# Kernel tuning notes

Hardware: AMD Instinct MI355X
Metric: run time of the kernel (lower is better)

Reference implementation:

```python
import jax, jax.numpy as jnp
import numpy as np

N_NODES = 50000
N_EDGES = 800000
N_GRAPHS = 512
NUM_TYPES = 1000
EMB = 128
HID = 128


def setup_inputs() -> dict:
    key = jax.random.key(0)
    ks = jax.random.split(key, 8)
    x_type = jax.random.randint(ks[0], (N_NODES,), 0, NUM_TYPES, dtype=jnp.int32)
    edge_index = jax.random.randint(ks[1], (2, N_EDGES), 0, N_NODES, dtype=jnp.int32)
    batch = jnp.sort(jax.random.randint(ks[2], (N_NODES,), 0, N_GRAPHS, dtype=jnp.int32))
    emb = jax.random.normal(ks[3], (NUM_TYPES, EMB), jnp.float32)
    s1 = 1.0 / np.sqrt(EMB)
    s2 = 1.0 / np.sqrt(HID)
    W1 = jax.random.normal(ks[4], (EMB, HID), jnp.float32) * s1
    b1 = jnp.zeros((HID,), jnp.float32)
    W2 = jax.random.normal(ks[5], (HID, HID), jnp.float32) * s2
    b2 = jnp.zeros((HID,), jnp.float32)
    return {"x_type": x_type, "edge_index": edge_index, "batch": batch,
            "emb": emb, "W1": W1, "b1": b1, "W2": W2, "b2": b2}


def _gcn_norm(edge_index, n_nodes):
    # PyG GCNConv default: add self-loops, symmetric normalization.
    loops = jnp.arange(n_nodes, dtype=edge_index.dtype)
    src = jnp.concatenate([edge_index[0], loops])  # [E+N]
    dst = jnp.concatenate([edge_index[1], loops])
    deg = jax.ops.segment_sum(jnp.ones_like(dst, jnp.float32), dst, num_segments=n_nodes)
    dis = jax.lax.rsqrt(deg)  # deg >= 1 thanks to self-loops
    norm = dis[src] * dis[dst]  # [E+N]
    return src, dst, norm


def _gcn_conv(x, src, dst, norm, W, b, n_nodes):
    h = x @ W                                  # [N, out]
    msg = h[src] * norm[:, None]               # edge-gathered, normalized messages
    out = jax.ops.segment_sum(msg, dst, num_segments=n_nodes)  # scatter-add
    return out + b


def reference(x_type, edge_index, batch, emb, W1, b1, W2, b2):
    src, dst, norm = _gcn_norm(edge_index, N_NODES)
    x = emb[x_type]                            # [N, EMB]
    x = jax.nn.relu(_gcn_conv(x, src, dst, norm, W1, b1, N_NODES))
    x = _gcn_conv(x, src, dst, norm, W2, b2, N_NODES)
    # index_add_ pooling over graphs (dropout is identity in eval / p=0)
    out = jax.ops.segment_sum(x, batch, num_segments=N_GRAPHS)  # [G, HID]
    return out
```

## Files before the change

### kernel.cpp

```cpp
#include <hip/hip_runtime.h>

#define N_NODES 50000
#define N_EDGES 800000
#define N_GRAPHS 512
#define FDIM 128
#define NTYPES_PAD 1000

#define NBLK 128
#define CHUNK ((N_EDGES + NBLK - 1) / NBLK)
#define NQUAD (N_NODES / 4)
#define NSB ((NQUAD + 255) / 256)
#define EMBW_BLOCKS 16
#define NPW 2
#define NW ((N_NODES + NPW - 1) / NPW)

typedef __bf16 bf16x8 __attribute__((ext_vector_type(8)));
typedef float f32x4 __attribute__((ext_vector_type(4)));
union BF8 { bf16x8 v; unsigned short u[8]; };

__device__ __forceinline__ unsigned short f2bf(float f) {
  unsigned int u = __float_as_uint(f);
  unsigned int r = (u + 0x7FFFu + ((u >> 16) & 1u)) >> 16;
  return (unsigned short)r;
}
__device__ __forceinline__ float bflo(unsigned int v) {
  return __uint_as_float(v << 16);
}
__device__ __forceinline__ float bfhi(unsigned int v) {
  return __uint_as_float(v & 0xFFFF0000u);
}

__global__ __launch_bounds__(512) void k_hist(const int* __restrict__ dst,
                                              unsigned int* __restrict__ Hist,
                                              unsigned char* __restrict__ rank8,
                                              int* __restrict__ g_done) {
  __shared__ unsigned int h[NQUAD];
  int b = blockIdx.x, t = threadIdx.x;
  if (b == 0 && t == 0) *g_done = 0;
  for (int i = t; i < NQUAD; i += 512) h[i] = 0;
  __syncthreads();
  int e0 = b * CHUNK, e1 = min(e0 + CHUNK, N_EDGES);
  for (int e = e0 + t; e < e1; e += 512) {
    int d = dst[e];
    unsigned int sh = (d & 3) * 8;
    unsigned int old = atomicAdd(&h[d >> 2], 1u << sh);
    rank8[e] = (unsigned char)((old >> sh) & 0xFFu);
  }
  __syncthreads();
  unsigned int* H = Hist + (size_t)b * NQUAD;
  for (int i = t; i < NQUAD; i += 512) H[i] = h[i];
}

__global__ __launch_bounds__(256) void k_prep(
    const unsigned int* __restrict__ Hist, const int* __restrict__ batch,
    unsigned int* __restrict__ Cur, float* __restrict__ dis,
    int* __restrict__ row_ptr, float* __restrict__ Zb,
    int* __restrict__ gstart, int* __restrict__ g_bsum,
    int* __restrict__ g_done, const float* __restrict__ emb,
    const float* __restrict__ W1, unsigned short* __restrict__ T1) {
  __shared__ unsigned short sh[16384];
  int blk = blockIdx.x, tid = threadIdx.x;

  if (blk >= NSB) {
    unsigned short* Ws = sh;
    int t = tid, w = t >> 6, l = t & 63;
    for (int i = t; i < 16384; i += 256) {
      int k = i >> 7, n = i & 127;
      Ws[n * 128 + (k ^ ((n & 15) << 3))] = f2bf(W1[i]);
    }
    int row0 = (blk - NSB) * 64 + w * 16;
    int arow = row0 + (l & 15);
    bool ok = arow < NTYPES_PAD;
    bf16x8 a[4];
#pragma unroll
    for (int ks = 0; ks < 4; ++ks) {
      BF8 av;
      const float* ap = emb + (size_t)arow * FDIM + (l >> 4) * 8 + ks * 32;
#pragma unroll
      for (int i = 0; i < 8; ++i) av.u[i] = ok ? f2bf(ap[i]) : 0;
      a[ks] = av.v;
    }
    __syncthreads();
    f32x4 acc[8] = {};
#pragma unroll
    for (int ks = 0; ks < 4; ++ks) {
#pragma unroll
      for (int ct = 0; ct < 8; ++ct) {
        int n = ct * 16 + (l & 15);
        int kk = (ks * 32 + (l >> 4) * 8) ^ ((n & 15) << 3);
        bf16x8 b = *(const bf16x8*)&Ws[n * 128 + kk];
        acc[ct] =
            __builtin_amdgcn_mfma_f32_16x16x32_bf16(a[ks], b, acc[ct], 0, 0, 0);
      }
    }
#pragma unroll
    for (int ct = 0; ct < 8; ++ct) {
      int col = ct * 16 + (l & 15);
#pragma unroll
      for (int r = 0; r < 4; ++r) {
        int row = row0 + (l >> 4) * 4 + r;
        if (row < NTYPES_PAD) T1[row * FDIM + col] = f2bf(acc[ct][r]);
      }
    }
    return;
  }

  int* si = (int*)sh;
  int q = blk * 256 + tid;

  for (int i = blk * 256 + tid; i < N_GRAPHS * FDIM; i += NSB * 256)
    Zb[i] = 0.0f;

  if (q < NQUAD) {
    int i0 = 4 * q;
    int prev = (i0 == 0) ? -1 : batch[i0 - 1];
#pragma unroll
    for (int k = 0; k < 4; ++k) {
      int i = i0 + k;
      int bb = batch[i];
      for (int g = prev + 1; g <= bb; ++g) gstart[g] = i;
      prev = bb;
    }
    if (i0 + 3 == N_NODES - 1)
      for (int g = prev + 1; g <= N_GRAPHS; ++g) gstart[g] = N_NODES;
  }

  unsigned int r0 = 0, r1 = 0, r2 = 0, r3 = 0;
  if (q < NQUAD) {
    for (int b = 0; b < NBLK; ++b) {
      unsigned int v = Hist[(size_t)b * NQUAD + q];
      Cur[(size_t)b * NQUAD + q] =
          (r0 & 255u) | ((r1 & 255u) << 8) | ((r2 & 255u) << 16) | (r3 << 24);
      r0 += v & 255u;
      r1 += (v >> 8) & 255u;
      r2 += (v >> 16) & 255u;
      r3 += v >> 24;
    }
    float4 dv = make_float4(rsqrtf((float)r0 + 1.f), rsqrtf((float)r1 + 1.f),
                            rsqrtf((float)r2 + 1.f), rsqrtf((float)r3 + 1.f));
    ((float4*)dis)[q] = dv;
  }

  int tsum = (q < NQUAD) ? (int)(r0 + r1 + r2 + r3) : 0;
  si[tid] = tsum;
  __syncthreads();
  for (int d = 1; d < 256; d <<= 1) {
    int u = (tid >= d) ? si[tid - d] : 0;
    __syncthreads();
    si[tid] += u;
    __syncthreads();
  }
  int excl = si[tid] - tsum;
  int btotal = si[255];

  if (tid == 0) {
    atomicExch(&g_bsum[blk], btotal);
    __threadfence();
    atomicAdd(g_done, 1);
    while (atomicAdd(g_done, 0) < NSB) {
    }
  }
  __syncthreads();
  int* sb = si + 256;
  if (tid < NSB) sb[tid] = atomicAdd(&g_bsum[tid], 0);
  __syncthreads();
  int bpref = 0;
  for (int t = 0; t < blk; ++t) bpref += sb[t];

  if (q < NQUAD) {
    int base = bpref + excl;
    ((int4*)row_ptr)[q] =
        make_int4(base, base + (int)r0, base + (int)(r0 + r1),
                  base + (int)(r0 + r1 + r2));
  }
  if (q == NQUAD - 1) row_ptr[N_NODES] = N_EDGES;
}

__global__ __launch_bounds__(512) void k_fill2(
    const int* __restrict__ src, const int* __restrict__ dst,
    const int* __restrict__ x_type, const int* __restrict__ row_ptr,
    const unsigned int* __restrict__ Cur, const unsigned char* __restrict__ rank8,
    const float* __restrict__ dis, unsigned long long* __restrict__ csr) {
  int e = blockIdx.x * blockDim.x + threadIdx.x;
  if (e >= N_EDGES) return;
  int b = e / CHUNK;
  int s = src[e], d = dst[e];
  unsigned int cw = Cur[(size_t)b * NQUAD + (d >> 2)];
  int base = (int)((cw >> ((d & 3) * 8)) & 0xFFu);
  int pos = row_ptr[d] + base + (int)rank8[e];
  unsigned int lo = (unsigned int)s | ((unsigned int)x_type[s] << 16);
  unsigned int hi = (unsigned int)f2bf(dis[d]);
  csr[pos] = (unsigned long long)lo | ((unsigned long long)hi << 32);
}

__global__ void k_agg1(const int* __restrict__ x_type,
                       const unsigned short* __restrict__ T1,
                       const float* __restrict__ b1,
                       const int* __restrict__ row_ptr,
                       const unsigned long long* __restrict__ csr,
                       const float* __restrict__ dis,
                       unsigned int* __restrict__ y1) {
  int gid = blockIdx.x * blockDim.x + threadIdx.x;
  int node = gid >> 6;
  int lane = gid & 63;
  if (node >= N_NODES) return;
  const unsigned int* T = (const unsigned int*)T1;
  const unsigned int* C = (const unsigned int*)csr;
  float di = dis[node];
  unsigned int v = T[(size_t)x_type[node] * 64 + lane];
  float ax = bflo(v) * di, ay = bfhi(v) * di;
  int j = row_ptr[node], end = row_ptr[node + 1];
  for (; j + 8 <= end; j += 8) {
    unsigned int e0 = C[2 * j], e1 = C[2 * j + 2];
    unsigned int e2 = C[2 * j + 4], e3 = C[2 * j + 6];
    unsigned int e4 = C[2 * j + 8], e5 = C[2 * j + 10];
    unsigned int e6 = C[2 * j + 12], e7 = C[2 * j + 14];
    unsigned int u0 = T[(size_t)(e0 >> 16) * 64 + lane];
    unsigned int u1 = T[(size_t)(e1 >> 16) * 64 + lane];
    unsigned int u2 = T[(size_t)(e2 >> 16) * 64 + lane];
    unsigned int u3 = T[(size_t)(e3 >> 16) * 64 + lane];
    unsigned int u4 = T[(size_t)(e4 >> 16) * 64 + lane];
    unsigned int u5 = T[(size_t)(e5 >> 16) * 64 + lane];
    unsigned int u6 = T[(size_t)(e6 >> 16) * 64 + lane];
    unsigned int u7 = T[(size_t)(e7 >> 16) * 64 + lane];
    float n0 = dis[e0 & 0xFFFFu], n1 = dis[e1 & 0xFFFFu];
    float n2 = dis[e2 & 0xFFFFu], n3 = dis[e3 & 0xFFFFu];
    float n4 = dis[e4 & 0xFFFFu], n5 = dis[e5 & 0xFFFFu];
    float n6 = dis[e6 & 0xFFFFu], n7 = dis[e7 & 0xFFFFu];
    ax = fmaf(bflo(u0), n0, ax); ay = fmaf(bfhi(u0), n0, ay);
    ax = fmaf(bflo(u1), n1, ax); ay = fmaf(bfhi(u1), n1, ay);
    ax = fmaf(bflo(u2), n2, ax); ay = fmaf(bfhi(u2), n2, ay);
    ax = fmaf(bflo(u3), n3, ax); ay = fmaf(bfhi(u3), n3, ay);
    ax = fmaf(bflo(u4), n4, ax); ay = fmaf(bfhi(u4), n4, ay);
    ax = fmaf(bflo(u5), n5, ax); ay = fmaf(bfhi(u5), n5, ay);
    ax = fmaf(bflo(u6), n6, ax); ay = fmaf(bfhi(u6), n6, ay);
    ax = fmaf(bflo(u7), n7, ax); ay = fmaf(bfhi(u7), n7, ay);
  }
  for (; j + 4 <= end; j += 4) {
    unsigned int e0 = C[2 * j], e1 = C[2 * j + 2];
    unsigned int e2 = C[2 * j + 4], e3 = C[2 * j + 6];
    unsigned int u0 = T[(size_t)(e0 >> 16) * 64 + lane];
    unsigned int u1 = T[(size_t)(e1 >> 16) * 64 + lane];
    unsigned int u2 = T[(size_t)(e2 >> 16) * 64 + lane];
    unsigned int u3 = T[(size_t)(e3 >> 16) * 64 + lane];
    float n0 = dis[e0 & 0xFFFFu], n1 = dis[e1 & 0xFFFFu];
    float n2 = dis[e2 & 0xFFFFu], n3 = dis[e3 & 0xFFFFu];
    ax = fmaf(bflo(u0), n0, ax); ay = fmaf(bfhi(u0), n0, ay);
    ax = fmaf(bflo(u1), n1, ax); ay = fmaf(bfhi(u1), n1, ay);
    ax = fmaf(bflo(u2), n2, ax); ay = fmaf(bfhi(u2), n2, ay);
    ax = fmaf(bflo(u3), n3, ax); ay = fmaf(bfhi(u3), n3, ay);
  }
  for (; j < end; ++j) {
    unsigned int e = C[2 * j];
    unsigned int u = T[(size_t)(e >> 16) * 64 + lane];
    float nw = dis[e & 0xFFFFu];
    ax = fmaf(bflo(u), nw, ax);
    ay = fmaf(bfhi(u), nw, ay);
  }
  float2 bb = ((const float2*)b1)[lane];
  ax = fmaxf(fmaf(di, ax, bb.x), 0.f) * di;
  ay = fmaxf(fmaf(di, ay, bb.y), 0.f) * di;
  y1[(size_t)node * 64 + lane] = (unsigned int)f2bf(ax) |
                                 ((unsigned int)f2bf(ay) << 16);
}

__global__ void k_aggpool(const unsigned int* __restrict__ y1,
                          const int* __restrict__ row_ptr,
                          const unsigned long long* __restrict__ csr,
                          const float* __restrict__ dis,
                          const int* __restrict__ batch,
                          float* __restrict__ Partials, int* __restrict__ Gid,
                          float* __restrict__ Zb) {
  int gid = blockIdx.x * blockDim.x + threadIdx.x;
  int wid = gid >> 6;
  int lane = gid & 63;
  int n0 = wid * NPW;
  if (n0 >= N_NODES) return;
  int nend = min(n0 + NPW, N_NODES);
  int g0 = batch[n0];
  float px = 0.f, py = 0.f;
  int node = n0;
  while (node < nend) {
    int g = batch[node];
    int rend = node + 1;
    while (rend < nend && batch[rend] == g) ++rend;
    float sx = 0.f, sy = 0.f;
    for (int n = node; n < rend; ++n) {
      float dn = dis[n];
      unsigned int v = y1[(size_t)n * 64 + lane];
      sx = fmaf(dn, bflo(v), sx);
      sy = fmaf(dn, bfhi(v), sy);
    }
    int j = row_ptr[node], jend = row_ptr[rend];
    for (; j + 16 <= jend; j += 16) {
#pragma unroll
      for (int k = 0; k < 16; ++k) {
        unsigned long long e = csr[j + k];
        unsigned int u = y1[(size_t)(e & 0xFFFFu) * 64 + lane];
        float w = __uint_as_float(((unsigned int)(e >> 32)) << 16);
        sx = fmaf(bflo(u), w, sx);
        sy = fmaf(bfhi(u), w, sy);
      }
    }
    for (; j + 4 <= jend; j += 4) {
#pragma unroll
      for (int k = 0; k < 4; ++k) {
        unsigned long long e = csr[j + k];
        unsigned int u = y1[(size_t)(e & 0xFFFFu) * 64 + lane];
        float w = __uint_as_float(((unsigned int)(e >> 32)) << 16);
        sx = fmaf(bflo(u), w, sx);
        sy = fmaf(bfhi(u), w, sy);
      }
    }
    for (; j < jend; ++j) {
      unsigned long long e = csr[j];
      unsigned int u = y1[(size_t)(e & 0xFFFFu) * 64 + lane];
      float w = __uint_as_float(((unsigned int)(e >> 32)) << 16);
      sx = fmaf(bflo(u), w, sx);
      sy = fmaf(bfhi(u), w, sy);
    }
    if (g == g0) {
      px += sx;
      py += sy;
    } else {
      atomicAdd(&Zb[(size_t)g * FDIM + 2 * lane], sx);
      atomicAdd(&Zb[(size_t)g * FDIM + 2 * lane + 1], sy);
    }
    node = rend;
  }
  ((float2*)Partials)[(size_t)wid * 64 + lane] = make_float2(px, py);
  if (lane == 0) Gid[wid] = g0;
}

__global__ __launch_bounds__(128) void k_poolzw2(
    const float* __restrict__ Partials, const int* __restrict__ Gid,
    const float* __restrict__ Zb, const int* __restrict__ gstart,
    const float* __restrict__ W2, const float* __restrict__ b2,
    float* __restrict__ out) {
  __shared__ float Zs[FDIM];
  int g = blockIdx.x, t = threadIdx.x;
  int s = gstart[g], e = gstart[g + 1];
  float acc = Zb[(size_t)g * FDIM + t];
  if (e > s) {
    int w0 = s / NPW, w1 = (e - 1) / NPW;
    for (int w = w0; w <= w1; ++w)
      if (Gid[w] == g) acc += Partials[(size_t)w * FDIM + t];
  }
  Zs[t] = acc;
  __syncthreads();
  float o = 0.f;
#pragma unroll 8
  for (int k = 0; k < FDIM; ++k) o = fmaf(Zs[k], W2[k * FDIM + t], o);
  out[(size_t)g * FDIM + t] = o + (float)(e - s) * b2[t];
}

extern "C" void kernel_launch(void* const* d_in, const int* in_sizes, int n_in,
                              void* d_out, int out_size, void* d_ws,
                              size_t ws_size, hipStream_t stream) {
  const int* x_type = (const int*)d_in[0];
  const int* edge_index = (const int*)d_in[1];
  const int* batch = (const int*)d_in[2];
  const float* emb = (const float*)d_in[3];
  const float* W1 = (const float*)d_in[4];
  const float* b1 = (const float*)d_in[5];
  const float* W2 = (const float*)d_in[6];
  const float* b2 = (const float*)d_in[7];
  float* out = (float*)d_out;

  const int* src = edge_index;
  const int* dst = edge_index + N_EDGES;

  char* p = (char*)d_ws;
  size_t off = 0;
  auto alloc = [&](size_t bytes) {
    void* r = p + off;
    off = (off + bytes + 255) & ~(size_t)255;
    return r;
  };
  float* dis = (float*)alloc(N_NODES * 4);
  int* row_ptr = (int*)alloc((N_NODES + 1) * 4);
  int* gstart = (int*)alloc((N_GRAPHS + 1) * 4);
  unsigned int* Hist = (unsigned int*)alloc((size_t)NBLK * NQUAD * 4);
  unsigned int* Cur = (unsigned int*)alloc((size_t)NBLK * NQUAD * 4);
  unsigned char* rank8 = (unsigned char*)alloc(N_EDGES);
  unsigned long long* csr =
      (unsigned long long*)alloc((size_t)N_EDGES * 8);
  unsigned short* T1 = (unsigned short*)alloc((size_t)NTYPES_PAD * FDIM * 2);
  unsigned int* y1 = (unsigned int*)alloc((size_t)N_NODES * 64 * 4);
  float* Partials = (float*)alloc((size_t)NW * FDIM * 4);
  int* Gid = (int*)alloc(NW * 4);
  float* Zb = (float*)alloc((size_t)N_GRAPHS * FDIM * 4);
  int* g_bsum = (int*)alloc(NSB * 4);
  int* g_done = (int*)alloc(4);
  (void)ws_size;

  k_hist<<<NBLK, 512, 0, stream>>>(dst, Hist, rank8, g_done);
  k_prep<<<NSB + EMBW_BLOCKS, 256, 0, stream>>>(
      Hist, batch, Cur, dis, row_ptr, Zb, gstart, g_bsum, g_done, emb, W1, T1);
  k_fill2<<<(N_EDGES + 511) / 512, 512, 0, stream>>>(
      src, dst, x_type, row_ptr, Cur, rank8, dis, csr);
  k_agg1<<<(N_NODES * 64 + 255) / 256, 256, 0, stream>>>(
      x_type, T1, b1, row_ptr, csr, dis, y1);
  k_aggpool<<<(NW * 64 + 255) / 256, 256, 0, stream>>>(
      y1, row_ptr, csr, dis, batch, Partials, Gid, Zb);
  k_poolzw2<<<N_GRAPHS, 128, 0, stream>>>(Partials, Gid, Zb, gstart, W2, b2,
                                          out);
}
```

Before: 148.3 us.

## Branchless padded edge loops, bf16 partials, and memset-based zero init

Replaces the unrolled-by-8/4/1 edge loops in both aggregation kernels with a single padded loop that clamps indices and zeroes weights past the row end. All gathers in a chunk are issued together and the remainder loops go away. Per-wave pooling partials are stored as packed bf16 instead of fp32, halving that traffic at some cost in precision. Zeroing of Zb and g_done moves from kernel code into hipMemsetAsync calls, which adds two extra stream operations.

```diff
diff --git a/kernel.cpp b/kernel.cpp
--- a/kernel.cpp
+++ b/kernel.cpp
@@ -32,11 +32,9 @@
 
 __global__ __launch_bounds__(512) void k_hist(const int* __restrict__ dst,
                                               unsigned int* __restrict__ Hist,
-                                              unsigned char* __restrict__ rank8,
-                                              int* __restrict__ g_done) {
+                                              unsigned char* __restrict__ rank8) {
   __shared__ unsigned int h[NQUAD];
   int b = blockIdx.x, t = threadIdx.x;
-  if (b == 0 && t == 0) *g_done = 0;
   for (int i = t; i < NQUAD; i += 512) h[i] = 0;
   __syncthreads();
   int e0 = b * CHUNK, e1 = min(e0 + CHUNK, N_EDGES);
@@ -54,10 +52,10 @@
 __global__ __launch_bounds__(256) void k_prep(
     const unsigned int* __restrict__ Hist, const int* __restrict__ batch,
     unsigned int* __restrict__ Cur, float* __restrict__ dis,
-    int* __restrict__ row_ptr, float* __restrict__ Zb,
-    int* __restrict__ gstart, int* __restrict__ g_bsum,
-    int* __restrict__ g_done, const float* __restrict__ emb,
-    const float* __restrict__ W1, unsigned short* __restrict__ T1) {
+    int* __restrict__ row_ptr, int* __restrict__ gstart,
+    int* __restrict__ g_bsum, int* __restrict__ g_done,
+    const float* __restrict__ emb, const float* __restrict__ W1,
+    unsigned short* __restrict__ T1) {
   __shared__ unsigned short sh[16384];
   int blk = blockIdx.x, tid = threadIdx.x;
 
@@ -107,9 +105,6 @@
 
   int* si = (int*)sh;
   int q = blk * 256 + tid;
-
-  for (int i = blk * 256 + tid; i < N_GRAPHS * FDIM; i += NSB * 256)
-    Zb[i] = 0.0f;
 
   if (q < NQUAD) {
     int i0 = 4 * q;
@@ -210,52 +205,23 @@
   unsigned int v = T[(size_t)x_type[node] * 64 + lane];
   float ax = bflo(v) * di, ay = bfhi(v) * di;
   int j = row_ptr[node], end = row_ptr[node + 1];
-  for (; j + 8 <= end; j += 8) {
-    unsigned int e0 = C[2 * j], e1 = C[2 * j + 2];
-    unsigned int e2 = C[2 * j + 4], e3 = C[2 * j + 6];
-    unsigned int e4 = C[2 * j + 8], e5 = C[2 * j + 10];
-    unsigned int e6 = C[2 * j + 12], e7 = C[2 * j + 14];
-    unsigned int u0 = T[(size_t)(e0 >> 16) * 64 + lane];
-    unsigned int u1 = T[(size_t)(e1 >> 16) * 64 + lane];
-    unsigned int u2 = T[(size_t)(e2 >> 16) * 64 + lane];
-    unsigned int u3 = T[(size_t)(e3 >> 16) * 64 + lane];
-    unsigned int u4 = T[(size_t)(e4 >> 16) * 64 + lane];
-    unsigned int u5 = T[(size_t)(e5 >> 16) * 64 + lane];
-    unsigned int u6 = T[(size_t)(e6 >> 16) * 64 + lane];
-    unsigned int u7 = T[(size_t)(e7 >> 16) * 64 + lane];
-    float n0 = dis[e0 & 0xFFFFu], n1 = dis[e1 & 0xFFFFu];
-    float n2 = dis[e2 & 0xFFFFu], n3 = dis[e3 & 0xFFFFu];
-    float n4 = dis[e4 & 0xFFFFu], n5 = dis[e5 & 0xFFFFu];
-    float n6 = dis[e6 & 0xFFFFu], n7 = dis[e7 & 0xFFFFu];
-    ax = fmaf(bflo(u0), n0, ax); ay = fmaf(bfhi(u0), n0, ay);
-    ax = fmaf(bflo(u1), n1, ax); ay = fmaf(bfhi(u1), n1, ay);
-    ax = fmaf(bflo(u2), n2, ax); ay = fmaf(bfhi(u2), n2, ay);
-    ax = fmaf(bflo(u3), n3, ax); ay = fmaf(bfhi(u3), n3, ay);
-    ax = fmaf(bflo(u4), n4, ax); ay = fmaf(bfhi(u4), n4, ay);
-    ax = fmaf(bflo(u5), n5, ax); ay = fmaf(bfhi(u5), n5, ay);
-    ax = fmaf(bflo(u6), n6, ax); ay = fmaf(bfhi(u6), n6, ay);
-    ax = fmaf(bflo(u7), n7, ax); ay = fmaf(bfhi(u7), n7, ay);
-  }
-  for (; j + 4 <= end; j += 4) {
-    unsigned int e0 = C[2 * j], e1 = C[2 * j + 2];
-    unsigned int e2 = C[2 * j + 4], e3 = C[2 * j + 6];
-    unsigned int u0 = T[(size_t)(e0 >> 16) * 64 + lane];
-    unsigned int u1 = T[(size_t)(e1 >> 16) * 64 + lane];
-    unsigned int u2 = T[(size_t)(e2 >> 16) * 64 + lane];
-    unsigned int u3 = T[(size_t)(e3 >> 16) * 64 + lane];
-    float n0 = dis[e0 & 0xFFFFu], n1 = dis[e1 & 0xFFFFu];
-    float n2 = dis[e2 & 0xFFFFu], n3 = dis[e3 & 0xFFFFu];
-    ax = fmaf(bflo(u0), n0, ax); ay = fmaf(bfhi(u0), n0, ay);
-    ax = fmaf(bflo(u1), n1, ax); ay = fmaf(bfhi(u1), n1, ay);
-    ax = fmaf(bflo(u2), n2, ax); ay = fmaf(bfhi(u2), n2, ay);
-    ax = fmaf(bflo(u3), n3, ax); ay = fmaf(bfhi(u3), n3, ay);
-  }
-  for (; j < end; ++j) {
-    unsigned int e = C[2 * j];
-    unsigned int u = T[(size_t)(e >> 16) * 64 + lane];
-    float nw = dis[e & 0xFFFFu];
-    ax = fmaf(bflo(u), nw, ax);
-    ay = fmaf(bfhi(u), nw, ay);
+  for (; j < end; j += 8) {
+    int lim = end - 1 - j;
+    unsigned int ee[8];
+#pragma unroll
+    for (int k = 0; k < 8; ++k) ee[k] = C[2 * (j + min(k, lim))];
+    unsigned int uu[8];
+#pragma unroll
+    for (int k = 0; k < 8; ++k) uu[k] = T[(size_t)(ee[k] >> 16) * 64 + lane];
+    float nn[8];
+#pragma unroll
+    for (int k = 0; k < 8; ++k)
+      nn[k] = (k <= lim) ? dis[ee[k] & 0xFFFFu] : 0.f;
+#pragma unroll
+    for (int k = 0; k < 8; ++k) {
+      ax = fmaf(bflo(uu[k]), nn[k], ax);
+      ay = fmaf(bfhi(uu[k]), nn[k], ay);
+    }
   }
   float2 bb = ((const float2*)b1)[lane];
   ax = fmaxf(fmaf(di, ax, bb.x), 0.f) * di;
@@ -269,8 +235,8 @@
                           const unsigned long long* __restrict__ csr,
                           const float* __restrict__ dis,
                           const int* __restrict__ batch,
-                          float* __restrict__ Partials, int* __restrict__ Gid,
-                          float* __restrict__ Zb) {
+                          unsigned int* __restrict__ Partials,
+                          int* __restrict__ Gid, float* __restrict__ Zb) {
   int gid = blockIdx.x * blockDim.x + threadIdx.x;
   int wid = gid >> 6;
   int lane = gid & 63;
@@ -292,32 +258,23 @@
       sy = fmaf(dn, bfhi(v), sy);
     }
     int j = row_ptr[node], jend = row_ptr[rend];
-    for (; j + 16 <= jend; j += 16) {
+    for (; j < jend; j += 16) {
+      int lim = jend - 1 - j;
+      unsigned long long ee[16];
+#pragma unroll
+      for (int k = 0; k < 16; ++k) ee[k] = csr[j + min(k, lim)];
+      unsigned int uu[16];
+#pragma unroll
+      for (int k = 0; k < 16; ++k)
+        uu[k] = y1[(size_t)(ee[k] & 0xFFFFu) * 64 + lane];
 #pragma unroll
       for (int k = 0; k < 16; ++k) {
-        unsigned long long e = csr[j + k];
-        unsigned int u = y1[(size_t)(e & 0xFFFFu) * 64 + lane];
-        float w = __uint_as_float(((unsigned int)(e >> 32)) << 16);
-        sx = fmaf(bflo(u), w, sx);
-        sy = fmaf(bfhi(u), w, sy);
+        float w = (k <= lim)
+                      ? __uint_as_float(((unsigned int)(ee[k] >> 32)) << 16)
+                      : 0.f;
+        sx = fmaf(bflo(uu[k]), w, sx);
+        sy = fmaf(bfhi(uu[k]), w, sy);
       }
-    }
-    for (; j + 4 <= jend; j += 4) {
-#pragma unroll
-      for (int k = 0; k < 4; ++k) {
-        unsigned long long e = csr[j + k];
-        unsigned int u = y1[(size_t)(e & 0xFFFFu) * 64 + lane];
-        float w = __uint_as_float(((unsigned int)(e >> 32)) << 16);
-        sx = fmaf(bflo(u), w, sx);
-        sy = fmaf(bfhi(u), w, sy);
-      }
-    }
-    for (; j < jend; ++j) {
-      unsigned long long e = csr[j];
-      unsigned int u = y1[(size_t)(e & 0xFFFFu) * 64 + lane];
-      float w = __uint_as_float(((unsigned int)(e >> 32)) << 16);
-      sx = fmaf(bflo(u), w, sx);
-      sy = fmaf(bfhi(u), w, sy);
     }
     if (g == g0) {
       px += sx;
@@ -328,12 +285,13 @@
     }
     node = rend;
   }
-  ((float2*)Partials)[(size_t)wid * 64 + lane] = make_float2(px, py);
+  Partials[(size_t)wid * 64 + lane] =
+      (unsigned int)f2bf(px) | ((unsigned int)f2bf(py) << 16);
   if (lane == 0) Gid[wid] = g0;
 }
 
 __global__ __launch_bounds__(128) void k_poolzw2(
-    const float* __restrict__ Partials, const int* __restrict__ Gid,
+    const unsigned int* __restrict__ Partials, const int* __restrict__ Gid,
     const float* __restrict__ Zb, const int* __restrict__ gstart,
     const float* __restrict__ W2, const float* __restrict__ b2,
     float* __restrict__ out) {
@@ -343,8 +301,12 @@
   float acc = Zb[(size_t)g * FDIM + t];
   if (e > s) {
     int w0 = s / NPW, w1 = (e - 1) / NPW;
+    int half = t & 1, pl = t >> 1;
     for (int w = w0; w <= w1; ++w)
-      if (Gid[w] == g) acc += Partials[(size_t)w * FDIM + t];
+      if (Gid[w] == g) {
+        unsigned int pv = Partials[(size_t)w * 64 + pl];
+        acc += half ? bfhi(pv) : bflo(pv);
+      }
   }
   Zs[t] = acc;
   __syncthreads();
@@ -387,16 +349,18 @@
       (unsigned long long*)alloc((size_t)N_EDGES * 8);
   unsigned short* T1 = (unsigned short*)alloc((size_t)NTYPES_PAD * FDIM * 2);
   unsigned int* y1 = (unsigned int*)alloc((size_t)N_NODES * 64 * 4);
-  float* Partials = (float*)alloc((size_t)NW * FDIM * 4);
+  unsigned int* Partials = (unsigned int*)alloc((size_t)NW * 64 * 4);
   int* Gid = (int*)alloc(NW * 4);
   float* Zb = (float*)alloc((size_t)N_GRAPHS * FDIM * 4);
   int* g_bsum = (int*)alloc(NSB * 4);
   int* g_done = (int*)alloc(4);
   (void)ws_size;
 
-  k_hist<<<NBLK, 512, 0, stream>>>(dst, Hist, rank8, g_done);
+  hipMemsetAsync(g_done, 0, 4, stream);
+  hipMemsetAsync(Zb, 0, (size_t)N_GRAPHS * FDIM * 4, stream);
+  k_hist<<<NBLK, 512, 0, stream>>>(dst, Hist, rank8);
   k_prep<<<NSB + EMBW_BLOCKS, 256, 0, stream>>>(
-      Hist, batch, Cur, dis, row_ptr, Zb, gstart, g_bsum, g_done, emb, W1, T1);
+      Hist, batch, Cur, dis, row_ptr, gstart, g_bsum, g_done, emb, W1, T1);
   k_fill2<<<(N_EDGES + 511) / 512, 512, 0, stream>>>(
       src, dst, x_type, row_ptr, Cur, rank8, dis, csr);
   k_agg1<<<(N_NODES * 64 + 255) / 256, 256, 0, stream>>>(
```

Measured after the change: 168.4 us. 13.5% more time.
